# Kernel tuning notes

Measured on AMD Instinct MI355X. Metric: run time of the kernel, lower is better.

## Reference

```python
import jax, jax.numpy as jnp
import numpy as np

N_NODES = 50000
N_EDGES = 800000
D = 64          # encoder output dim (encoder.out)
MLP_DIM = 64    # mlp_edge_model hidden dim


def setup_inputs() -> dict:
    key = jax.random.key(0)
    ks = jax.random.split(key, 8)
    x = jax.random.normal(ks[0], (N_NODES, D), dtype=jnp.float32)
    edge_index = jax.random.randint(ks[1], (2, N_EDGES), 0, N_NODES, dtype=jnp.int64)
    # xavier-ish scaled weights
    W_enc = jax.random.normal(ks[2], (D, D), dtype=jnp.float32) * (1.0 / np.sqrt(D))
    b_enc = jnp.zeros((D,), dtype=jnp.float32)
    W1 = jax.random.normal(ks[3], (2 * D, MLP_DIM), dtype=jnp.float32) * (1.0 / np.sqrt(2 * D))
    b1 = jnp.zeros((MLP_DIM,), dtype=jnp.float32)
    W2 = jax.random.normal(ks[4], (MLP_DIM, 1), dtype=jnp.float32) * (1.0 / np.sqrt(MLP_DIM))
    b2 = jnp.zeros((1,), dtype=jnp.float32)
    return {"x": x, "edge_index": edge_index, "W_enc": W_enc, "b_enc": b_enc,
            "W1": W1, "b1": b1, "W2": W2, "b2": b2}


def reference(x, edge_index, W_enc, b_enc, W1, b1, W2, b2):
    src, dst = edge_index[0], edge_index[1]
    # --- encoder: 1-layer message-passing GCN stand-in ---
    agg = jax.ops.segment_sum(x[src], dst, num_segments=N_NODES)   # [N, D]
    node_emb = jax.nn.relu((x + agg) @ W_enc + b_enc)              # [N, D]
    # --- gather src/dst embeddings, concat, 2-layer MLP edge scorer ---
    edge_emb = jnp.concatenate([node_emb[src], node_emb[dst]], axis=1)  # [E, 2D]
    h = jax.nn.relu(edge_emb @ W1 + b1)                            # [E, mlp_dim]
    edge_logits = h @ W2 + b2                                      # [E, 1]
    return edge_logits
```

## Files before the change

### kernel.cpp

```cpp
#include <hip/hip_runtime.h>
#include <hip/hip_bf16.h>
#include <stdint.h>

#define N_NODES 50000
#define N_EDGES 800000
#define D 64
#define VROWS 50048
#define CVT_BLOCKS 3125
#define CAP 64

typedef __hip_bfloat16 bf16;
typedef __bf16 bf16x8 __attribute__((ext_vector_type(8)));
typedef float  f32x4  __attribute__((ext_vector_type(4)));

__device__ __forceinline__ float bu2f(unsigned short u) {
    unsigned int w = ((unsigned int)u) << 16;
    return __builtin_bit_cast(float, w);
}
__device__ __forceinline__ unsigned short f2bu(float f) {
    bf16 h = __float2bfloat16(f);
    return __builtin_bit_cast(unsigned short, h);
}
__device__ __forceinline__ float ldf(const void* p, size_t i, bool f32mode) {
    if (f32mode) return ((const float*)p)[i];
    return bu2f(((const unsigned short*)p)[i]);
}
__device__ __forceinline__ void stf(void* p, size_t i, float v, bool f32mode) {
    if (f32mode) ((float*)p)[i] = v;
    else ((unsigned short*)p)[i] = f2bu(v);
}
__device__ __forceinline__ int ldidx(const int* ei, size_t e, int row, bool i64mode) {
    if (i64mode) return ei[((size_t)row * N_EDGES + e) * 2];
    return ei[(size_t)row * N_EDGES + e];
}
__device__ __forceinline__ void unpack8(uint4 v, float* f) {
    f[0] = bu2f(v.x & 0xffff); f[1] = bu2f(v.x >> 16);
    f[2] = bu2f(v.y & 0xffff); f[3] = bu2f(v.y >> 16);
    f[4] = bu2f(v.z & 0xffff); f[5] = bu2f(v.z >> 16);
    f[6] = bu2f(v.w & 0xffff); f[7] = bu2f(v.w >> 16);
}

__global__ __launch_bounds__(256) void init_kernel(
    const void* __restrict__ x, const int* __restrict__ ei,
    const void* __restrict__ W2, const void* __restrict__ b1,
    const void* __restrict__ b2,
    int* __restrict__ flags, unsigned short* __restrict__ w2bf,
    float* __restrict__ b1f, float* __restrict__ b2fp,
    int* __restrict__ counts,
    unsigned short* __restrict__ xbf)
{
    __shared__ int sh_f32m, sh_i64m;
    int tid = threadIdx.x;

    if (tid < 64) {
        const unsigned short* u = (const unsigned short*)x;
        int weird = 0, zeros = 0;
        #pragma unroll
        for (int k = tid; k < 128; k += 64) {
            int ex = (u[2 * k] >> 7) & 0xFF;
            if (ex < 90 || ex > 160) ++weird;
            if (ei[2 * k + 1] == 0) ++zeros;
        }
        #pragma unroll
        for (int off = 1; off < 64; off <<= 1) {
            weird += __shfl_xor(weird, off, 64);
            zeros += __shfl_xor(zeros, off, 64);
        }
        if (tid == 0) {
            sh_f32m = (weird > 32) ? 1 : 0;
            sh_i64m = (zeros > 120) ? 1 : 0;
        }
    }
    __syncthreads();
    bool f32m = sh_f32m != 0;

    if (blockIdx.x == 0) {
        if (tid < 64) {
            w2bf[tid] = f2bu(ldf(W2, tid, f32m));
            b1f[tid]  = ldf(b1, tid, f32m);
        }
        if (tid == 0) {
            flags[0] = f32m ? 1 : 0;
            flags[1] = sh_i64m;
            b2fp[0] = ldf(b2, 0, f32m);
        }
    }

    int cbase = blockIdx.x * 16 + (tid & 15);
    if (tid < 16 && cbase < N_NODES) counts[cbase] = 0;

    size_t idx4 = (size_t)blockIdx.x * 256 + tid;
    if (f32m) {
        float4 fv = ((const float4*)x)[idx4];
        ushort4 o;
        o.x = f2bu(fv.x); o.y = f2bu(fv.y); o.z = f2bu(fv.z); o.w = f2bu(fv.w);
        ((ushort4*)xbf)[idx4] = o;
    } else {
        ((uint2*)xbf)[idx4] = ((const uint2*)x)[idx4];
    }
}

__global__ __launch_bounds__(256) void histfill_kernel(
    const int* __restrict__ ei, int* __restrict__ counts,
    unsigned short* __restrict__ sarr, int* __restrict__ earr,
    const int* __restrict__ flags)
{
    bool i64m = flags[1] != 0;
    int grp   = blockIdx.x & 7;
    int e = (blockIdx.x >> 3) * 256 + threadIdx.x;
    if (e >= N_EDGES) return;
    int d = ldidx(ei, e, 1, i64m);
    if (((d >> 6) & 7) != grp) return;
    int s = ldidx(ei, e, 0, i64m);
    int r = atomicAdd(&counts[d], 1);
    if (r < CAP) {
        int pos = d * CAP + r;
        sarr[pos] = (unsigned short)s;
        earr[pos] = e;
    }
}

__global__ __launch_bounds__(256) void gather_kernel(
    const unsigned short* __restrict__ xbf,
    const int* __restrict__ counts, const unsigned short* __restrict__ sarr,
    unsigned short* __restrict__ vtab)
{
    int w    = (blockIdx.x * 256 + threadIdx.x) >> 6;
    int lane = threadIdx.x & 63;
    if (w >= N_NODES) return;
    int cnt = counts[w];
    if (cnt > CAP) cnt = CAP;
    int beg = w * CAP, end = beg + cnt;
    int f8   = lane & 7;
    int slot = lane >> 3;

    float acc[8] = {0.f, 0.f, 0.f, 0.f, 0.f, 0.f, 0.f, 0.f};
    if (slot == 0) {
        uint4 q = ((const uint4*)xbf)[(size_t)w * 8 + f8];
        unpack8(q, acc);
    }

    int j = beg;
    for (; j + 16 <= end; j += 16) {
        int s0 = sarr[j + slot];
        int s1 = sarr[j + 8 + slot];
        uint4 q0 = ((const uint4*)xbf)[(size_t)s0 * 8 + f8];
        uint4 q1 = ((const uint4*)xbf)[(size_t)s1 * 8 + f8];
        float f0[8], f1[8];
        unpack8(q0, f0);
        unpack8(q1, f1);
        #pragma unroll
        for (int i = 0; i < 8; ++i) acc[i] += f0[i] + f1[i];
    }
    for (; j < end; j += 8) {
        int e = j + slot;
        bool ok = e < end;
        int s = sarr[ok ? e : beg];
        uint4 q = ((const uint4*)xbf)[(size_t)s * 8 + f8];
        float f[8];
        unpack8(q, f);
        if (ok) {
            #pragma unroll
            for (int i = 0; i < 8; ++i) acc[i] += f[i];
        }
    }

    #pragma unroll
    for (int i = 0; i < 8; ++i) {
        acc[i] += __shfl_xor(acc[i], 8, 64);
        acc[i] += __shfl_xor(acc[i], 16, 64);
        acc[i] += __shfl_xor(acc[i], 32, 64);
    }

    if (slot == 0) {
        uint4 o;
        o.x = (unsigned int)f2bu(acc[0]) | ((unsigned int)f2bu(acc[1]) << 16);
        o.y = (unsigned int)f2bu(acc[2]) | ((unsigned int)f2bu(acc[3]) << 16);
        o.z = (unsigned int)f2bu(acc[4]) | ((unsigned int)f2bu(acc[5]) << 16);
        o.w = (unsigned int)f2bu(acc[6]) | ((unsigned int)f2bu(acc[7]) << 16);
        ((uint4*)vtab)[(size_t)w * 8 + f8] = o;
    }
}

__global__ __launch_bounds__(256) void nodemm_kernel(
    const unsigned short* vtab,
    const void* __restrict__ W_enc, const void* __restrict__ b_enc,
    const void* __restrict__ W1,
    unsigned short* p_src, unsigned short* p_dst,
    const float* __restrict__ b1f, const int* __restrict__ flags)
{
    __shared__ unsigned short wtWe[64 * 72];
    __shared__ unsigned short wtWa[64 * 72];
    __shared__ unsigned short wtWb[64 * 72];
    __shared__ float benc[64];
    __shared__ unsigned short ebuf[4][16 * 72];

    bool f32m = flags[0] != 0;
    int tid = threadIdx.x;
    for (int t = tid; t < 4096; t += 256) {
        int i = t >> 6, j = t & 63;
        wtWe[j * 72 + i] = f2bu(ldf(W_enc, t, f32m));
        wtWa[j * 72 + i] = f2bu(ldf(W1, t, f32m));
        wtWb[j * 72 + i] = f2bu(ldf(W1, 4096 + t, f32m));
    }
    if (tid < 64) benc[tid] = ldf(b_enc, tid, f32m);
    __syncthreads();

    int wave = tid >> 6;
    int lane = tid & 63;
    int lo   = lane & 15;
    int quad = lane >> 4;
    unsigned short* eb = ebuf[wave];
    int base = blockIdx.x * 64 + wave * 16;

    bf16x8 av0 = *(const bf16x8*)&vtab[(size_t)(base + lo) * D + quad * 8];
    bf16x8 av1 = *(const bf16x8*)&vtab[(size_t)(base + lo) * D + 32 + quad * 8];

    f32x4 z = {0.f, 0.f, 0.f, 0.f};
    f32x4 acc1[4] = {z, z, z, z};
    #pragma unroll
    for (int nt = 0; nt < 4; ++nt) {
        bf16x8 b0  = *(const bf16x8*)&wtWe[(nt * 16 + lo) * 72 + quad * 8];
        bf16x8 b1v = *(const bf16x8*)&wtWe[(nt * 16 + lo) * 72 + 32 + quad * 8];
        acc1[nt] = __builtin_amdgcn_mfma_f32_16x16x32_bf16(av0, b0, acc1[nt], 0, 0, 0);
        acc1[nt] = __builtin_amdgcn_mfma_f32_16x16x32_bf16(av1, b1v, acc1[nt], 0, 0, 0);
    }
    #pragma unroll
    for (int nt = 0; nt < 4; ++nt) {
        float bias = benc[nt * 16 + lo];
        #pragma unroll
        for (int r = 0; r < 4; ++r) {
            int m = quad * 4 + r;
            float ev = fmaxf(acc1[nt][r] + bias, 0.f);
            eb[m * 72 + nt * 16 + lo] = f2bu(ev);
        }
    }

    bf16x8 ae0 = *(const bf16x8*)&eb[lo * 72 + quad * 8];
    bf16x8 ae1 = *(const bf16x8*)&eb[lo * 72 + 32 + quad * 8];

    f32x4 acc2[4] = {z, z, z, z};
    f32x4 acc3[4] = {z, z, z, z};
    #pragma unroll
    for (int nt = 0; nt < 4; ++nt) {
        bf16x8 ba0 = *(const bf16x8*)&wtWa[(nt * 16 + lo) * 72 + quad * 8];
        bf16x8 ba1 = *(const bf16x8*)&wtWa[(nt * 16 + lo) * 72 + 32 + quad * 8];
        bf16x8 bb0 = *(const bf16x8*)&wtWb[(nt * 16 + lo) * 72 + quad * 8];
        bf16x8 bb1 = *(const bf16x8*)&wtWb[(nt * 16 + lo) * 72 + 32 + quad * 8];
        acc2[nt] = __builtin_amdgcn_mfma_f32_16x16x32_bf16(ae0, ba0, acc2[nt], 0, 0, 0);
        acc2[nt] = __builtin_amdgcn_mfma_f32_16x16x32_bf16(ae1, ba1, acc2[nt], 0, 0, 0);
        acc3[nt] = __builtin_amdgcn_mfma_f32_16x16x32_bf16(ae0, bb0, acc3[nt], 0, 0, 0);
        acc3[nt] = __builtin_amdgcn_mfma_f32_16x16x32_bf16(ae1, bb1, acc3[nt], 0, 0, 0);
    }
    #pragma unroll
    for (int nt = 0; nt < 4; ++nt) {
        float b1v = b1f[nt * 16 + lo];
        #pragma unroll
        for (int r = 0; r < 4; ++r) {
            int node = base + quad * 4 + r;
            if (node < N_NODES) {
                size_t idx = (size_t)node * D + nt * 16 + lo;
                p_src[idx] = f2bu(acc2[nt][r] + b1v);
                p_dst[idx] = f2bu(acc3[nt][r]);
            }
        }
    }
}

__global__ __launch_bounds__(256) void edge_kernel(
    const unsigned short* __restrict__ p_src,
    const unsigned short* __restrict__ p_dst,
    const int* __restrict__ counts,
    const unsigned short* __restrict__ sarr, const int* __restrict__ earr,
    const unsigned short* __restrict__ w2bf, const float* __restrict__ b2fp,
    void* __restrict__ out, const int* __restrict__ flags)
{
    bool f32m = flags[0] != 0;
    int w    = (blockIdx.x * 256 + threadIdx.x) >> 6;
    int lane = threadIdx.x & 63;
    if (w >= N_NODES) return;
    int cnt = counts[w];
    if (cnt > CAP) cnt = CAP;
    if (cnt == 0) return;
    int beg = w * CAP, end = beg + cnt;

    int sub = lane & 7;
    int g   = lane >> 3;

    uint4 pdv = ((const uint4*)p_dst)[(size_t)w * 8 + sub];
    uint4 w2v = ((const uint4*)w2bf)[sub];
    float pd[8], w2[8];
    unpack8(pdv, pd);
    unpack8(w2v, w2);
    float bb = b2fp[0];

    int j = beg;
    for (; j + 16 <= end; j += 16) {
        int p0 = j + g, p1 = j + 8 + g;
        int s0 = sarr[p0];
        int s1 = sarr[p1];
        uint4 q0 = ((const uint4*)p_src)[(size_t)s0 * 8 + sub];
        uint4 q1 = ((const uint4*)p_src)[(size_t)s1 * 8 + sub];
        float f0[8], f1[8];
        unpack8(q0, f0);
        unpack8(q1, f1);
        float c0 = 0.f, c1 = 0.f;
        #pragma unroll
        for (int i = 0; i < 8; ++i) {
            c0 += fmaxf(f0[i] + pd[i], 0.f) * w2[i];
            c1 += fmaxf(f1[i] + pd[i], 0.f) * w2[i];
        }
        c0 += __shfl_xor(c0, 1, 64);
        c0 += __shfl_xor(c0, 2, 64);
        c0 += __shfl_xor(c0, 4, 64);
        c1 += __shfl_xor(c1, 1, 64);
        c1 += __shfl_xor(c1, 2, 64);
        c1 += __shfl_xor(c1, 4, 64);
        if (sub == 0) {
            stf(out, earr[p0], c0 + bb, f32m);
            stf(out, earr[p1], c1 + bb, f32m);
        }
    }
    for (; j < end; j += 8) {
        int pos = j + g;
        bool ok = pos < end;
        int idx = ok ? pos : beg;
        int s = sarr[idx];
        uint4 psv = ((const uint4*)p_src)[(size_t)s * 8 + sub];
        float ps[8];
        unpack8(psv, ps);
        float c = 0.f;
        #pragma unroll
        for (int i = 0; i < 8; ++i)
            c += fmaxf(ps[i] + pd[i], 0.f) * w2[i];
        c += __shfl_xor(c, 1, 64);
        c += __shfl_xor(c, 2, 64);
        c += __shfl_xor(c, 4, 64);
        if (sub == 0 && ok) {
            int eid = earr[pos];
            stf(out, eid, c + bb, f32m);
        }
    }
}

extern "C" void kernel_launch(void* const* d_in, const int* in_sizes, int n_in,
                              void* d_out, int out_size, void* d_ws, size_t ws_size,
                              hipStream_t stream)
{
    const void* x     = d_in[0];
    const int*  ei    = (const int*)d_in[1];
    const void* W_enc = d_in[2];
    const void* b_enc = d_in[3];
    const void* W1    = d_in[4];
    const void* b1    = d_in[5];
    const void* W2    = d_in[6];
    const void* b2    = d_in[7];

    const size_t NTv  = (size_t)VROWS * D;
    const size_t NCAP = (size_t)N_NODES * CAP;
    unsigned short* p_src = (unsigned short*)d_ws;
    unsigned short* p_dst = p_src + NTv;
    unsigned short* xbf   = p_dst + NTv;
    unsigned short* sarr  = xbf + NTv;
    int*   earr    = (int*)(sarr + NCAP);
    float* b1f     = (float*)(earr + NCAP);
    unsigned short* w2bf = (unsigned short*)(b1f + 64);
    float* b2fp    = (float*)(w2bf + 64);
    int*   counts  = (int*)(b2fp + 4);
    int*   flags   = counts + N_NODES;

    unsigned short* vtab = p_src;

    init_kernel<<<CVT_BLOCKS, 256, 0, stream>>>(x, ei, W2, b1, b2, flags, w2bf,
                                                b1f, b2fp, counts, xbf);

    const int EB8 = ((N_EDGES + 255) / 256) * 8;
    histfill_kernel<<<EB8, 256, 0, stream>>>(ei, counts, sarr, earr, flags);

    const int NWB = (N_NODES * 64 + 255) / 256;
    gather_kernel<<<NWB, 256, 0, stream>>>(xbf, counts, sarr, vtab);
    nodemm_kernel<<<(N_NODES + 63) / 64, 256, 0, stream>>>(vtab, W_enc, b_enc, W1,
                                                           p_src, p_dst, b1f, flags);
    edge_kernel<<<NWB, 256, 0, stream>>>(p_src, p_dst, counts, sarr, earr,
                                         w2bf, b2fp, d_out, flags);
}
```

Before: 189.0 us.

## Compact edge indices to u16 in init and pack src/edge-id pairs

The init kernel now converts the edge index array into compact 16-bit src/dst arrays, so the 8-pass histfill kernel reads 2-byte indices instead of re-reading the full int32/int64 edge_index on every pass. The separate sarr/earr CSR arrays are merged into one interleaved uint2 array, so the edge kernel gets the source node and edge id with a single 8-byte load. The gather kernel now reads 8 bytes per entry where it used to read 2, which raises its index traffic. The 16-bit truncation relies on node ids being below 65536, and init writes dst16/src16 over the full 3125x256 grid, which matches N_EDGES exactly.

```diff
diff --git a/kernel.cpp b/kernel.cpp
--- a/kernel.cpp
+++ b/kernel.cpp
@@ -47,7 +47,8 @@
     int* __restrict__ flags, unsigned short* __restrict__ w2bf,
     float* __restrict__ b1f, float* __restrict__ b2fp,
     int* __restrict__ counts,
-    unsigned short* __restrict__ xbf)
+    unsigned short* __restrict__ xbf,
+    unsigned short* __restrict__ dst16, unsigned short* __restrict__ src16)
 {
     __shared__ int sh_f32m, sh_i64m;
     int tid = threadIdx.x;
@@ -73,6 +74,7 @@
     }
     __syncthreads();
     bool f32m = sh_f32m != 0;
+    bool i64m = sh_i64m != 0;
 
     if (blockIdx.x == 0) {
         if (tid < 64) {
@@ -88,6 +90,10 @@
 
     int cbase = blockIdx.x * 16 + (tid & 15);
     if (tid < 16 && cbase < N_NODES) counts[cbase] = 0;
+
+    int e = blockIdx.x * 256 + tid;
+    dst16[e] = (unsigned short)ldidx(ei, e, 1, i64m);
+    src16[e] = (unsigned short)ldidx(ei, e, 0, i64m);
 
     size_t idx4 = (size_t)blockIdx.x * 256 + tid;
     if (f32m) {
@@ -101,28 +107,27 @@
 }
 
 __global__ __launch_bounds__(256) void histfill_kernel(
-    const int* __restrict__ ei, int* __restrict__ counts,
-    unsigned short* __restrict__ sarr, int* __restrict__ earr,
-    const int* __restrict__ flags)
-{
-    bool i64m = flags[1] != 0;
-    int grp   = blockIdx.x & 7;
+    const unsigned short* __restrict__ dst16,
+    const unsigned short* __restrict__ src16,
+    int* __restrict__ counts, uint2* __restrict__ epack)
+{
+    int grp = blockIdx.x & 7;
     int e = (blockIdx.x >> 3) * 256 + threadIdx.x;
     if (e >= N_EDGES) return;
-    int d = ldidx(ei, e, 1, i64m);
+    int d = dst16[e];
     if (((d >> 6) & 7) != grp) return;
-    int s = ldidx(ei, e, 0, i64m);
     int r = atomicAdd(&counts[d], 1);
     if (r < CAP) {
-        int pos = d * CAP + r;
-        sarr[pos] = (unsigned short)s;
-        earr[pos] = e;
+        uint2 v;
+        v.x = (unsigned int)src16[e];
+        v.y = (unsigned int)e;
+        epack[(size_t)d * CAP + r] = v;
     }
 }
 
 __global__ __launch_bounds__(256) void gather_kernel(
     const unsigned short* __restrict__ xbf,
-    const int* __restrict__ counts, const unsigned short* __restrict__ sarr,
+    const int* __restrict__ counts, const uint2* __restrict__ epack,
     unsigned short* __restrict__ vtab)
 {
     int w    = (blockIdx.x * 256 + threadIdx.x) >> 6;
@@ -142,8 +147,8 @@
 
     int j = beg;
     for (; j + 16 <= end; j += 16) {
-        int s0 = sarr[j + slot];
-        int s1 = sarr[j + 8 + slot];
+        int s0 = (int)epack[j + slot].x;
+        int s1 = (int)epack[j + 8 + slot].x;
         uint4 q0 = ((const uint4*)xbf)[(size_t)s0 * 8 + f8];
         uint4 q1 = ((const uint4*)xbf)[(size_t)s1 * 8 + f8];
         float f0[8], f1[8];
@@ -155,7 +160,7 @@
     for (; j < end; j += 8) {
         int e = j + slot;
         bool ok = e < end;
-        int s = sarr[ok ? e : beg];
+        int s = (int)epack[ok ? e : beg].x;
         uint4 q = ((const uint4*)xbf)[(size_t)s * 8 + f8];
         float f[8];
         unpack8(q, f);
@@ -271,7 +276,7 @@
     const unsigned short* __restrict__ p_src,
     const unsigned short* __restrict__ p_dst,
     const int* __restrict__ counts,
-    const unsigned short* __restrict__ sarr, const int* __restrict__ earr,
+    const uint2* __restrict__ epack,
     const unsigned short* __restrict__ w2bf, const float* __restrict__ b2fp,
     void* __restrict__ out, const int* __restrict__ flags)
 {
@@ -297,10 +302,10 @@
     int j = beg;
     for (; j + 16 <= end; j += 16) {
         int p0 = j + g, p1 = j + 8 + g;
-        int s0 = sarr[p0];
-        int s1 = sarr[p1];
-        uint4 q0 = ((const uint4*)p_src)[(size_t)s0 * 8 + sub];
-        uint4 q1 = ((const uint4*)p_src)[(size_t)s1 * 8 + sub];
+        uint2 e0 = epack[p0];
+        uint2 e1 = epack[p1];
+        uint4 q0 = ((const uint4*)p_src)[(size_t)e0.x * 8 + sub];
+        uint4 q1 = ((const uint4*)p_src)[(size_t)e1.x * 8 + sub];
         float f0[8], f1[8];
         unpack8(q0, f0);
         unpack8(q1, f1);
@@ -317,16 +322,15 @@
         c1 += __shfl_xor(c1, 2, 64);
         c1 += __shfl_xor(c1, 4, 64);
         if (sub == 0) {
-            stf(out, earr[p0], c0 + bb, f32m);
-            stf(out, earr[p1], c1 + bb, f32m);
+            stf(out, e0.y, c0 + bb, f32m);
+            stf(out, e1.y, c1 + bb, f32m);
         }
     }
     for (; j < end; j += 8) {
         int pos = j + g;
         bool ok = pos < end;
-        int idx = ok ? pos : beg;
-        int s = sarr[idx];
-        uint4 psv = ((const uint4*)p_src)[(size_t)s * 8 + sub];
+        uint2 ev = epack[ok ? pos : beg];
+        uint4 psv = ((const uint4*)p_src)[(size_t)ev.x * 8 + sub];
         float ps[8];
         unpack8(psv, ps);
         float c = 0.f;
@@ -337,8 +341,7 @@
         c += __shfl_xor(c, 2, 64);
         c += __shfl_xor(c, 4, 64);
         if (sub == 0 && ok) {
-            int eid = earr[pos];
-            stf(out, eid, c + bb, f32m);
+            stf(out, ev.y, c + bb, f32m);
         }
     }
 }
@@ -361,26 +364,28 @@
     unsigned short* p_src = (unsigned short*)d_ws;
     unsigned short* p_dst = p_src + NTv;
     unsigned short* xbf   = p_dst + NTv;
-    unsigned short* sarr  = xbf + NTv;
-    int*   earr    = (int*)(sarr + NCAP);
-    float* b1f     = (float*)(earr + NCAP);
+    uint2* epack   = (uint2*)(xbf + NTv);
+    float* b1f     = (float*)(epack + NCAP);
     unsigned short* w2bf = (unsigned short*)(b1f + 64);
     float* b2fp    = (float*)(w2bf + 64);
     int*   counts  = (int*)(b2fp + 4);
     int*   flags   = counts + N_NODES;
+    unsigned short* dst16 = (unsigned short*)(flags + 2);
+    unsigned short* src16 = dst16 + N_EDGES;
 
     unsigned short* vtab = p_src;
 
     init_kernel<<<CVT_BLOCKS, 256, 0, stream>>>(x, ei, W2, b1, b2, flags, w2bf,
-                                                b1f, b2fp, counts, xbf);
+                                                b1f, b2fp, counts, xbf,
+                                                dst16, src16);
 
     const int EB8 = ((N_EDGES + 255) / 256) * 8;
-    histfill_kernel<<<EB8, 256, 0, stream>>>(ei, counts, sarr, earr, flags);
+    histfill_kernel<<<EB8, 256, 0, stream>>>(dst16, src16, counts, epack);
 
     const int NWB = (N_NODES * 64 + 255) / 256;
-    gather_kernel<<<NWB, 256, 0, stream>>>(xbf, counts, sarr, vtab);
+    gather_kernel<<<NWB, 256, 0, stream>>>(xbf, counts, epack, vtab);
     nodemm_kernel<<<(N_NODES + 63) / 64, 256, 0, stream>>>(vtab, W_enc, b_enc, W1,
                                                            p_src, p_dst, b1f, flags);
-    edge_kernel<<<NWB, 256, 0, stream>>>(p_src, p_dst, counts, sarr, earr,
+    edge_kernel<<<NWB, 256, 0, stream>>>(p_src, p_dst, counts, epack,
                                          w2bf, b2fp, d_out, flags);
 }
```

Measured after the change: 189.3 us. Within noise of the previous version (+0.1%).
